# Optimization experiments

Hardware: AMD Instinct MI355X
Metric: run time of the kernel (lower is better)

The kernel has to match this reference:

```python
import jax, jax.numpy as jnp
from jax import lax
import numpy as np

B, N, F_IN, T = 8, 2048, 2, 12
K, F_CHEV, F_TIME = 3, 64, 64
LN_EPS = 1e-5


def _cheb_polys(key):
    # random symmetric row-normalized 'scaled Laplacian' proxy, then Chebyshev recurrence
    A = jax.random.uniform(key, (N, N), dtype=jnp.float32)
    A = (A + A.T) * 0.5
    A = A / A.sum(axis=1, keepdims=True)
    L = A - jnp.eye(N, dtype=jnp.float32)  # eigenvalues roughly in [-1, 1]
    Ts = [jnp.eye(N, dtype=jnp.float32), L]
    for _ in range(2, K):
        Ts.append(2.0 * L @ Ts[-1] - Ts[-2])
    return jnp.stack(Ts[:K])  # (K, N, N)


def setup_inputs() -> dict:
    key = jax.random.key(0)
    ks = jax.random.split(key, 20)
    g = lambda i, s: jax.random.normal(ks[i], s, dtype=jnp.float32)
    xav = lambda i, s: g(i, s) * np.sqrt(2.0 / (s[-2] + s[-1]))
    return {
        "x": g(0, (B, N, F_IN, T)),
        "cheb": _cheb_polys(ks[1]),
        "Theta": xav(2, (K, F_IN, F_CHEV)),
        # temporal attention params
        "U1": g(3, (N,)), "U2": xav(4, (F_IN, N)), "U3": g(5, (F_IN,)),
        "be": g(6, (1, T, T)) * 0.1, "Ve": xav(7, (T, T)),
        # spatial attention params
        "W1": g(8, (T,)), "W2": xav(9, (F_IN, T)), "W3": g(10, (F_IN,)),
        "bs": g(11, (1, N, N)) * 0.1, "Vs": xav(12, (N, N)),
        # convs + layernorm
        "tconv_w": g(13, (F_TIME, F_CHEV, 1, 3)) * np.sqrt(2.0 / (F_CHEV * 3 + F_TIME)),
        "tconv_b": jax.random.uniform(ks[14], (F_TIME,), dtype=jnp.float32),
        "rconv_w": g(15, (F_TIME, F_IN, 1, 1)) * np.sqrt(2.0 / (F_IN + F_TIME)),
        "rconv_b": jax.random.uniform(ks[16], (F_TIME,), dtype=jnp.float32),
        "ln_g": jnp.ones((F_TIME,), jnp.float32),
        "ln_b": jnp.zeros((F_TIME,), jnp.float32),
    }


def _forward(x, cheb, Theta, U1, U2, U3, be, Ve, W1, W2, W3, bs, Vs,
             tconv_w, tconv_b, rconv_w, rconv_b, ln_g, ln_b):
    b, n, f, t = x.shape
    # ---- temporal attention: (B,T,T) ----
    lhs_t = jnp.einsum('bnft,n->btf', x, U1) @ U2          # (B,T,N)
    rhs_t = jnp.einsum('f,bnft->bnt', U3, x)               # (B,N,T)
    prod_t = jnp.einsum('btn,bnu->btu', lhs_t, rhs_t)      # (B,T,T)
    E = jnp.einsum('tu,buv->btv', Ve, jax.nn.sigmoid(prod_t + be))
    E = jax.nn.softmax(E, axis=1)
    # apply temporal attention
    x_TAt = (x.reshape(b, n * f, t) @ E).reshape(b, n, f, t)
    # ---- spatial attention: (B,N,N) ----
    lhs_s = jnp.einsum('bnft,t->bnf', x_TAt, W1) @ W2      # (B,N,T)
    rhs_s = jnp.einsum('f,bnft->btn', W3, x_TAt)           # (B,T,N)
    prod_s = jnp.einsum('bnt,btm->bnm', lhs_s, rhs_s)      # (B,N,N)
    S = jnp.einsum('mn,bnp->bmp', Vs, jax.nn.sigmoid(prod_s + bs))
    S = jax.nn.softmax(S, axis=1)
    # ---- Chebyshev graph conv with spatial attention (vectorized over k, t) ----
    # rhs[b,k,n,f,t] = sum_m (cheb[k,m,n] * S[b,m,n]) * x[b,m,f,t]
    rhs = jnp.einsum('kmn,bmn,bmft->bknft', cheb, S, x)
    gcn = jax.nn.relu(jnp.einsum('bknft,kfo->bnot', rhs, Theta))  # (B,N,F_chev,T)
    # ---- time conv (1x3, pad 1 along T) + 1x1 residual conv ----
    dn = ('NCHW', 'OIHW', 'NCHW')
    tc = lax.conv_general_dilated(gcn.transpose(0, 2, 1, 3), tconv_w, (1, 1),
                                  ((0, 0), (1, 1)), dimension_numbers=dn)
    tc = tc + tconv_b[None, :, None, None]                 # (B,F_time,N,T)
    res = lax.conv_general_dilated(x.transpose(0, 2, 1, 3), rconv_w, (1, 1),
                                   ((0, 0), (0, 0)), dimension_numbers=dn)
    res = res + rconv_b[None, :, None, None]
    y = jax.nn.relu(res + tc).transpose(0, 3, 2, 1)        # (B,T,N,F_time)
    mu = y.mean(-1, keepdims=True)
    var = jnp.mean((y - mu) ** 2, axis=-1, keepdims=True)
    y = (y - mu) * lax.rsqrt(var + LN_EPS) * ln_g + ln_b
    return y.transpose(0, 2, 3, 1)                          # (B,N,F_time,T)


def reference(x, cheb, Theta, U1, U2, U3, be, Ve, W1, W2, W3, bs, Vs,
              tconv_w, tconv_b, rconv_w, rconv_b, ln_g, ln_b):
    return _forward(x, cheb, Theta, U1, U2, U3, be, Ve, W1, W2, W3, bs, Vs,
                    tconv_w, tconv_b, rconv_w, rconv_b, ln_g, ln_b)
```

## Files before the change

### kernel.cpp

```cpp
#include <hip/hip_runtime.h>
#include <cstdint>
#include <cstddef>

#define NB 8
#define NN 2048
#define MCV 16

using bf16x8 = __attribute__((ext_vector_type(8))) __bf16;
using f32x4  = __attribute__((ext_vector_type(4))) float;

__device__ __forceinline__ float bf2f(unsigned short u) {
  union { unsigned int i; float f; } v; v.i = ((unsigned int)u) << 16; return v.f;
}
__device__ __forceinline__ unsigned short f2bf(float f) {
  union { float f; unsigned int i; } v; v.f = f;
  unsigned int lsb = (v.i >> 16) & 1u;
  v.i += 0x7fffu + lsb;
  return (unsigned short)(v.i >> 16);
}
__device__ __forceinline__ float ld_in(const void* p, size_t idx, int mode) {
  return mode ? bf2f(((const unsigned short*)p)[idx]) : ((const float*)p)[idx];
}
__device__ __forceinline__ int get_mode(const void* chebp) {
  return ((const unsigned int*)chebp)[0] != 0x3F800000u;
}

#define GLOAD16(gptr, lptr) \
  __builtin_amdgcn_global_load_lds((const __attribute__((address_space(1))) void*)(gptr), \
                                   (__attribute__((address_space(3))) void*)(lptr), 16, 0, 0)

struct Seg { const void* src; void* dst; int count; int tobf; };
struct ConvArgs { Seg s[16]; };

__global__ void k_convert(ConvArgs a, const void* __restrict__ chebp) {
  const int mode = get_mode(chebp);
  const int stride = gridDim.x * blockDim.x;
  for (int si = 0; si < 16; ++si) {
    const Seg sg = a.s[si];
    for (int i = blockIdx.x * blockDim.x + threadIdx.x; i < sg.count; i += stride) {
      float v = ld_in(sg.src, i, mode);
      if (sg.tobf) ((unsigned short*)sg.dst)[i] = f2bf(v);
      else         ((float*)sg.dst)[i] = v;
    }
  }
}

__global__ void k_vsb(const void* __restrict__ vs, unsigned short* __restrict__ out,
                      const void* __restrict__ tw, unsigned short* __restrict__ twr,
                      const void* __restrict__ chebp) {
  const int mode = get_mode(chebp);
  const int idx = blockIdx.x * 256 + threadIdx.x;
  if (idx < NN * NN) {
    const int ke = idx & 7, row = (idx >> 3) & 127, kc = (idx >> 10) & 7;
    const int hf = (idx >> 13) & 1, kt = (idx >> 14) & 31, mt = idx >> 19;
    const int m = mt * 256 + hf * 128 + row, k = kt * 64 + kc * 8 + ke;
    out[idx] = f2bf(ld_in(vs, (size_t)m * NN + k, mode));
  } else {
    const int j = idx - NN * NN;
    if (j < 12288) {
      const int dt = j >> 12, rem = j & 4095, o = rem >> 6, c = rem & 63;
      twr[j] = f2bf(ld_in(tw, (size_t)o * 192 + c * 3 + dt, mode));
    }
  }
}

__global__ __launch_bounds__(256) void k_temp1(const float* __restrict__ xf,
      const float* __restrict__ U1f, const float* __restrict__ U2f, const float* __restrict__ U3f,
      const float* __restrict__ bef, const float* __restrict__ Vef, float* __restrict__ E) {
  const int b = blockIdx.x;
  float accL[24], accG[24];
#pragma unroll
  for (int i = 0; i < 24; i++) { accL[i] = 0.f; accG[i] = 0.f; }
  const float u30 = U3f[0], u31 = U3f[1];
  for (int n = threadIdx.x; n < NN; n += 256) {
    const float* xp = xf + ((size_t)b * NN + n) * 24;
    const float u1 = U1f[n], u20 = U2f[n], u21 = U2f[NN + n];
#pragma unroll
    for (int t = 0; t < 12; t++) {
      float x0 = xp[t], x1 = xp[12 + t];
      accL[t * 2 + 0] += u1 * x0;
      accL[t * 2 + 1] += u1 * x1;
      float xs = u30 * x0 + u31 * x1;
      accG[t]      += u20 * xs;
      accG[12 + t] += u21 * xs;
    }
  }
#pragma unroll
  for (int i = 0; i < 24; i++) {
#pragma unroll
    for (int d = 32; d >= 1; d >>= 1) {
      accL[i] += __shfl_xor(accL[i], d, 64);
      accG[i] += __shfl_xor(accG[i], d, 64);
    }
  }
  __shared__ float red[4][48];
  __shared__ float L[48];
  __shared__ float s0[12][12], e1[12][12];
  const int lane = threadIdx.x & 63, wv = threadIdx.x >> 6;
  if (lane == 0) {
#pragma unroll
    for (int i = 0; i < 24; i++) { red[wv][i] = accL[i]; red[wv][24 + i] = accG[i]; }
  }
  __syncthreads();
  if (threadIdx.x < 48)
    L[threadIdx.x] = red[0][threadIdx.x] + red[1][threadIdx.x]
                   + red[2][threadIdx.x] + red[3][threadIdx.x];
  __syncthreads();
  const int tid = threadIdx.x;
  const int t = tid / 12, v = tid % 12;
  if (tid < 144) {
    float pr = L[t * 2 + 0] * L[24 + v] + L[t * 2 + 1] * L[36 + v] + bef[t * 12 + v];
    s0[t][v] = 1.f / (1.f + __expf(-pr));
  }
  __syncthreads();
  if (tid < 144) {
    float s = 0.f;
#pragma unroll
    for (int u = 0; u < 12; u++) s += Vef[t * 12 + u] * s0[u][v];
    e1[t][v] = s;
  }
  __syncthreads();
  if (tid < 144) {
    float mx = -1e30f;
#pragma unroll
    for (int u = 0; u < 12; u++) mx = fmaxf(mx, e1[u][v]);
    float sm = 0.f;
#pragma unroll
    for (int u = 0; u < 12; u++) sm += __expf(e1[u][v] - mx);
    E[b * 144 + t * 12 + v] = __expf(e1[t][v] - mx) / sm;
  }
}

__global__ __launch_bounds__(256) void k_xtat(const float* __restrict__ xf,
      const float* __restrict__ E, const float* __restrict__ W1f, const float* __restrict__ W2f,
      const float* __restrict__ W3f, float* __restrict__ lhs, float* __restrict__ rhsS) {
  const int b = blockIdx.y;
  const int n = blockIdx.x * 256 + threadIdx.x;
  __shared__ float Es[144];
  if (threadIdx.x < 144) Es[threadIdx.x] = E[b * 144 + threadIdx.x];
  __syncthreads();
  const float* xp = xf + ((size_t)b * NN + n) * 24;
  float xv[24];
#pragma unroll
  for (int i = 0; i < 24; i++) xv[i] = xp[i];
  float xT[24];
#pragma unroll
  for (int f = 0; f < 2; f++)
#pragma unroll
    for (int v = 0; v < 12; v++) {
      float s = 0.f;
#pragma unroll
      for (int u = 0; u < 12; u++) s += xv[f * 12 + u] * Es[u * 12 + v];
      xT[f * 12 + v] = s;
    }
  float a0 = 0.f, a1 = 0.f;
#pragma unroll
  for (int v = 0; v < 12; v++) { a0 += xT[v] * W1f[v]; a1 += xT[12 + v] * W1f[v]; }
  const float w30 = W3f[0], w31 = W3f[1];
  float* lp = lhs + ((size_t)b * NN + n) * 12;
#pragma unroll
  for (int t = 0; t < 12; t++) {
    lp[t] = a0 * W2f[t] + a1 * W2f[12 + t];
    rhsS[((size_t)b * 12 + t) * NN + n] = w30 * xT[t] + w31 * xT[12 + t];
  }
}

__global__ __launch_bounds__(256) void k_sig(const float* __restrict__ lhs,
      const float* __restrict__ rhsS, const void* __restrict__ bs,
      unsigned short* __restrict__ sigT, const void* __restrict__ chebp, int p0, int PL) {
  const int tid = threadIdx.x;
  const int n = blockIdx.x * 256 + tid;
  const int pg0 = p0 + blockIdx.y * 16;
  const int mode = get_mode(chebp);
  __shared__ float rsl[8][12][16];
  for (int i = tid; i < 1536; i += 256) {
    int b = i / 192, t = (i % 192) / 16, c = i % 16;
    rsl[b][t][c] = rhsS[((size_t)b * 12 + t) * NN + pg0 + c];
  }
  float bsv[16];
  if (mode) {
    const int4* bp = (const int4*)((const unsigned short*)bs + (size_t)n * NN + pg0);
    int4 q0 = bp[0], q1 = bp[1];
    const unsigned short* u0 = (const unsigned short*)&q0;
    const unsigned short* u1 = (const unsigned short*)&q1;
#pragma unroll
    for (int i = 0; i < 8; i++) { bsv[i] = bf2f(u0[i]); bsv[8 + i] = bf2f(u1[i]); }
  } else {
    const float4* fp = (const float4*)((const float*)bs + (size_t)n * NN + pg0);
#pragma unroll
    for (int q = 0; q < 4; q++) {
      float4 v = fp[q];
      bsv[q * 4 + 0] = v.x; bsv[q * 4 + 1] = v.y; bsv[q * 4 + 2] = v.z; bsv[q * 4 + 3] = v.w;
    }
  }
  __syncthreads();
  const size_t kpart = (size_t)(n >> 6) * 16384 + (size_t)((n >> 3) & 7) * 1024 + (n & 7);
  const int plbase = pg0 - p0;
  for (int b = 0; b < 8; b++) {
    float lv[12];
    const float* lp = lhs + ((size_t)b * NN + n) * 12;
#pragma unroll
    for (int t = 0; t < 12; t++) lv[t] = lp[t];
    const int gbase = b * PL + plbase;
    const size_t gt_off = (size_t)(gbase >> 8) * 524288 + (size_t)((gbase >> 7) & 1) * 8192
                        + (size_t)(gbase & 127) * 8;
#pragma unroll
    for (int pp = 0; pp < 16; pp++) {
      float acc = bsv[pp];
#pragma unroll
      for (int t = 0; t < 12; t++) acc += lv[t] * rsl[b][t][pp];
      float sg = 1.f / (1.f + __expf(-acc));
      sigT[gt_off + (size_t)pp * 8 + kpart] = f2bf(sg);
    }
  }
}

__global__ __launch_bounds__(512, 2) void k_gemm(const unsigned short* __restrict__ A,
      const unsigned short* __restrict__ Bm, unsigned short* __restrict__ C,
      float* __restrict__ pmax, float* __restrict__ psum,
      int PL, int plshift, int GP, int nwg) {
  __shared__ __align__(16) unsigned short lA[2][16384];
  __shared__ __align__(16) unsigned short lB[2][16384];
  const int id = blockIdx.x;
  const int cpx = nwg >> 3;
  const int sid = (id & 7) * cpx + (id >> 3);
  const int s = sid >> 4, w = sid & 15;
  const int mt = (s & 1) * 4 + (w & 3);
  const int pt = (s >> 1) * 4 + (w >> 2);
  const int tid = threadIdx.x;
  const int wv = tid >> 6, lane = tid & 63;
  const int fr = lane & 15, hi = lane >> 4;
  const int wr = wv >> 2, wc = wv & 3;
  const unsigned short* gA = A  + (size_t)mt * 524288;
  const unsigned short* gB = Bm + (size_t)pt * 524288;

  f32x4 acc[8][4] = {};
  bf16x8 af[8][2], bfr[4][2];

#define STAGE_H(h) do { \
    const int kt_ = (h) >> 2, part_ = (h) & 3, r_ = part_ & 1; \
    const unsigned short* gsrc_ = ((part_ < 2) ? gA : gB) + (size_t)kt_ * 16384 + r_ * 8192 + tid * 8; \
    unsigned short* ldst_ = ((part_ < 2) ? &lA[0][0] : &lB[0][0]) + (kt_ & 1) * 16384 + r_ * 8192 + wv * 512; \
    GLOAD16(gsrc_,        ldst_); \
    GLOAD16(gsrc_ + 4096, ldst_ + 4096); \
  } while (0)

#define READ_A(bf) do { \
    _Pragma("unroll") for (int mi_ = 0; mi_ < 8; ++mi_) \
    _Pragma("unroll") for (int s2_ = 0; s2_ < 2; ++s2_) \
      af[mi_][s2_] = *(const bf16x8*)&lA[bf][wr * 8192 + (s2_ * 4 + hi) * 1024 + (mi_ * 16 + fr) * 8]; \
  } while (0)

#define READ_B(bf) do { \
    _Pragma("unroll") for (int ni_ = 0; ni_ < 4; ++ni_) \
    _Pragma("unroll") for (int s2_ = 0; s2_ < 2; ++s2_) \
      bfr[ni_][s2_] = *(const bf16x8*)&lB[bf][(wc >> 1) * 8192 + (s2_ * 4 + hi) * 1024 \
                                             + ((wc & 1) * 64 + ni_ * 16 + fr) * 8]; \
  } while (0)

#define MFMA_Q(mh, nh) do { \
    __builtin_amdgcn_s_setprio(1); \
    _Pragma("unroll") for (int s2_ = 0; s2_ < 2; ++s2_) \
    _Pragma("unroll") for (int mi_ = 0; mi_ < 4; ++mi_) \
    _Pragma("unroll") for (int ni_ = 0; ni_ < 2; ++ni_) \
      acc[(mh) * 4 + mi_][(nh) * 2 + ni_] = __builtin_amdgcn_mfma_f32_16x16x32_bf16( \
          af[(mh) * 4 + mi_][s2_], bfr[(nh) * 2 + ni_][s2_], acc[(mh) * 4 + mi_][(nh) * 2 + ni_], 0, 0, 0); \
    __builtin_amdgcn_s_setprio(0); \
  } while (0)

#define PH_BAR() __builtin_amdgcn_s_barrier()
#define PH_LGKM() asm volatile("s_waitcnt lgkmcnt(0)" ::: "memory")

  for (int h = 0; h < 8; ++h) STAGE_H(h);
  asm volatile("s_waitcnt vmcnt(8)" ::: "memory");
  PH_BAR();

#pragma unroll 1
  for (int i = 0; i < 16; ++i) {
    const int hb = 8 * i;
    const bool more = (i < 15);
    READ_A(0); READ_B(0);
    if (i > 0) STAGE_H(hb + 7);
    PH_BAR(); PH_LGKM();
    MFMA_Q(0, 0);
    PH_BAR();
    if (more) STAGE_H(hb + 8);
    PH_BAR(); PH_LGKM();
    MFMA_Q(0, 1);
    PH_BAR();
    if (more) STAGE_H(hb + 9);
    PH_BAR(); PH_LGKM();
    MFMA_Q(1, 0);
    PH_BAR();
    if (more) STAGE_H(hb + 10);
    PH_BAR(); PH_LGKM();
    MFMA_Q(1, 1);
    if (more) asm volatile("s_waitcnt vmcnt(6)" ::: "memory");
    else      asm volatile("s_waitcnt vmcnt(0)" ::: "memory");
    PH_BAR();
    READ_A(1); READ_B(1);
    if (more) STAGE_H(hb + 11);
    PH_BAR(); PH_LGKM();
    MFMA_Q(0, 0);
    PH_BAR();
    if (more) STAGE_H(hb + 12);
    PH_BAR(); PH_LGKM();
    MFMA_Q(0, 1);
    PH_BAR();
    if (more) STAGE_H(hb + 13);
    PH_BAR(); PH_LGKM();
    MFMA_Q(1, 0);
    PH_BAR();
    if (more) STAGE_H(hb + 14);
    PH_BAR(); PH_LGKM();
    MFMA_Q(1, 1);
    if (more) asm volatile("s_waitcnt vmcnt(6)" ::: "memory");
    else      asm volatile("s_waitcnt vmcnt(0)" ::: "memory");
    PH_BAR();
  }
#undef STAGE_H
#undef READ_A
#undef READ_B
#undef MFMA_Q
#undef PH_BAR
#undef PH_LGKM

  const int m0 = mt * 256, gcol0 = pt * 256;
  const int plmask = PL - 1;
#pragma unroll
  for (int ni = 0; ni < 4; ++ni) {
    float lmax = -1e30f;
    float vr[8][4];
#pragma unroll
    for (int mi = 0; mi < 8; ++mi) {
      const int g = gcol0 + wc * 64 + ni * 16 + fr;
      const int b = g >> plshift, pl = g & plmask;
      const int mrow = m0 + wr * 128 + mi * 16 + hi * 4;
      unsigned short* cp = C + ((size_t)b * NN + mrow) * PL + pl;
#pragma unroll
      for (int r = 0; r < 4; r++) {
        unsigned short us = f2bf(acc[mi][ni][r]);
        cp[(size_t)r * PL] = us;
        vr[mi][r] = bf2f(us);
        lmax = fmaxf(lmax, vr[mi][r]);
      }
    }
    float lsum = 0.f;
#pragma unroll
    for (int mi = 0; mi < 8; ++mi)
#pragma unroll
      for (int r = 0; r < 4; r++) lsum += __expf(vr[mi][r] - lmax);
#pragma unroll
    for (int d = 16; d <= 32; d <<= 1) {
      float omax = __shfl_xor(lmax, d, 64);
      float osum = __shfl_xor(lsum, d, 64);
      float nm = fmaxf(lmax, omax);
      lsum = lsum * __expf(lmax - nm) + osum * __expf(omax - nm);
      lmax = nm;
    }
    if (hi == 0) {
      const int part = mt * 2 + wr;
      const int g = gcol0 + wc * 64 + ni * 16 + lane;
      pmax[(size_t)part * GP + g] = lmax;
      psum[(size_t)part * GP + g] = lsum;
    }
  }
}

__global__ __launch_bounds__(256) void k_cheb(const unsigned short* __restrict__ S0c,
        const void* __restrict__ cheb, const unsigned short* __restrict__ cbf, int use_cbf,
        const float* __restrict__ xf, const float* __restrict__ pmax, const float* __restrict__ psum,
        float* __restrict__ part, int p0, int PL, int mspan, int GP) {
  const int b = blockIdx.z, mc = blockIdx.y;
  const int pl = blockIdx.x * 256 + threadIdx.x;
  const int n = p0 + pl;
  const int mode = get_mode(cheb);
  const int g = b * PL + pl;
  float mx = -1e30f;
#pragma unroll
  for (int c = 0; c < 16; c++) mx = fmaxf(mx, pmax[(size_t)c * GP + g]);
  float sm = 0.f;
#pragma unroll
  for (int c = 0; c < 16; c++) sm += psum[(size_t)c * GP + g] * __expf(pmax[(size_t)c * GP + g] - mx);
  const float inv = 1.f / sm;
  float acc[3][24];
#pragma unroll
  for (int k = 0; k < 3; k++)
#pragma unroll
    for (int j = 0; j < 24; j++) acc[k][j] = 0.f;
  const unsigned short* s0p = S0c + (size_t)b * NN * PL + pl;
  const int mEnd = mc * mspan + mspan;
  if (use_cbf || mode) {
    const unsigned short* cb = (use_cbf ? cbf : (const unsigned short*)cheb) + n;
#pragma unroll 2
    for (int m = mc * mspan; m < mEnd; ++m) {
      float w = __expf(bf2f(s0p[(size_t)m * PL]) - mx) * inv;
      const f32x4* xp = (const f32x4*)(xf + ((size_t)b * NN + m) * 24);
      float w0 = w * bf2f(cb[(size_t)m * NN]);
      float w1 = w * bf2f(cb[(size_t)NN * NN + (size_t)m * NN]);
      float w2 = w * bf2f(cb[(size_t)2 * NN * NN + (size_t)m * NN]);
#pragma unroll
      for (int q = 0; q < 6; q++) {
        f32x4 xv = xp[q];
#pragma unroll
        for (int e = 0; e < 4; e++) {
          int j = q * 4 + e;
          acc[0][j] += w0 * xv[e];
          acc[1][j] += w1 * xv[e];
          acc[2][j] += w2 * xv[e];
        }
      }
    }
  } else {
    const float* cb = (const float*)cheb + n;
#pragma unroll 2
    for (int m = mc * mspan; m < mEnd; ++m) {
      float w = __expf(bf2f(s0p[(size_t)m * PL]) - mx) * inv;
      const f32x4* xp = (const f32x4*)(xf + ((size_t)b * NN + m) * 24);
      float w0 = w * cb[(size_t)m * NN];
      float w1 = w * cb[(size_t)NN * NN + (size_t)m * NN];
      float w2 = w * cb[(size_t)2 * NN * NN + (size_t)m * NN];
#pragma unroll
      for (int q = 0; q < 6; q++) {
        f32x4 xv = xp[q];
#pragma unroll
        for (int e = 0; e < 4; e++) {
          int j = q * 4 + e;
          acc[0][j] += w0 * xv[e];
          acc[1][j] += w1 * xv[e];
          acc[2][j] += w2 * xv[e];
        }
      }
    }
  }
  float* pp = part + ((size_t)(mc * 8 + b) * 72) * PL + pl;
#pragma unroll
  for (int k = 0; k < 3; k++)
#pragma unroll
    for (int j = 0; j < 24; j++) pp[(size_t)(k * 24 + j) * PL] = acc[k][j];
}

__global__ void k_chebred(const float* __restrict__ part, float* __restrict__ rhsC,
                          int p0, int PL) {
  const int idx = blockIdx.x * 256 + threadIdx.x;
  if (idx >= 8 * 72 * PL) return;
  const int pl = idx % PL;
  const int r = idx / PL;
  const int j = r % 72, b = r / 72;
  float s = 0.f;
  for (int mc = 0; mc < MCV; ++mc)
    s += part[((size_t)(mc * 8 + b) * 72 + j) * PL + pl];
  rhsC[((size_t)b * NN + p0 + pl) * 72 + j] = s;
}

__global__ __launch_bounds__(256) void k_final(const float* __restrict__ rhsC,
      const float* __restrict__ Thf, const unsigned short* __restrict__ twr,
      const float* __restrict__ tbf, const float* __restrict__ rwf, const float* __restrict__ rbf,
      const float* __restrict__ lngf, const float* __restrict__ lnbf,
      const float* __restrict__ xf, void* __restrict__ out, const void* __restrict__ chebp) {
  const int mode = get_mode(chebp);
  __shared__ __align__(16) unsigned short ltw[192 * 72];
  __shared__ __align__(16) unsigned short gT[4][18][72];
  __shared__ float rl[4][72];
  __shared__ float prm[6][64];
  const int tid = threadIdx.x;
  const int wv = tid >> 6, lane = tid & 63;
  const size_t bn = (size_t)blockIdx.x * 4 + wv;

  for (int i = tid; i < 1536; i += 256) {
    const int row = i >> 3, cseg = (i & 7) * 8;
    *(bf16x8*)&ltw[row * 72 + cseg] = *(const bf16x8*)&twr[row * 64 + cseg];
  }
  if (tid < 64) {
    prm[0][tid] = tbf[tid] + rbf[tid];
    prm[1][tid] = rwf[tid * 2];
    prm[2][tid] = rwf[tid * 2 + 1];
    prm[3][tid] = lngf[tid];
    prm[4][tid] = lnbf[tid];
  }
  for (int i = lane; i < 648; i += 64) ((unsigned int*)&gT[wv][0][0])[i] = 0u;
  {
    const float* rp = rhsC + bn * 72;
    rl[wv][lane] = rp[lane];
    if (lane < 8) rl[wv][64 + lane] = rp[64 + lane];
  }
  __syncthreads();
  {
    const int c = lane;
    float th[6];
#pragma unroll
    for (int kf = 0; kf < 6; kf++) th[kf] = Thf[kf * 64 + c];
#pragma unroll
    for (int t = 0; t < 12; t++) {
      float s = 0.f;
#pragma unroll
      for (int kf = 0; kf < 6; kf++) s += rl[wv][kf * 12 + t] * th[kf];
      gT[wv][1 + t][c] = f2bf(fmaxf(s, 0.f));
    }
  }
  __syncthreads();
  const int fr = lane & 15, hi = lane >> 4;
  f32x4 acc4[4] = {};
#pragma unroll
  for (int dt = 0; dt < 3; dt++)
#pragma unroll
    for (int ks = 0; ks < 2; ks++) {
      bf16x8 bfrag = *(const bf16x8*)&gT[wv][fr + dt][ks * 32 + hi * 8];
#pragma unroll
      for (int ot = 0; ot < 4; ot++) {
        bf16x8 afrag = *(const bf16x8*)&ltw[(dt * 64 + ot * 16 + fr) * 72 + ks * 32 + hi * 8];
        acc4[ot] = __builtin_amdgcn_mfma_f32_16x16x32_bf16(afrag, bfrag, acc4[ot], 0, 0, 0);
      }
    }
  const int t = fr;
  const int tc = t < 12 ? t : 11;
  const float x0 = xf[bn * 24 + tc], x1 = xf[bn * 24 + 12 + tc];
  float vals[4][4];
  float sum = 0.f, sumsq = 0.f;
#pragma unroll
  for (int ot = 0; ot < 4; ot++) {
    f32x4 rbt4 = *(const f32x4*)&prm[0][ot * 16 + hi * 4];
    f32x4 rw04 = *(const f32x4*)&prm[1][ot * 16 + hi * 4];
    f32x4 rw14 = *(const f32x4*)&prm[2][ot * 16 + hi * 4];
#pragma unroll
    for (int r = 0; r < 4; r++) {
      float v = acc4[ot][r] + rbt4[r] + rw04[r] * x0 + rw14[r] * x1;
      v = fmaxf(v, 0.f);
      vals[ot][r] = v;
      sum += v; sumsq += v * v;
    }
  }
  sum   += __shfl_xor(sum, 16, 64);
  sumsq += __shfl_xor(sumsq, 16, 64);
  sum   += __shfl_xor(sum, 32, 64);
  sumsq += __shfl_xor(sumsq, 32, 64);
  const float mu = sum * (1.f / 64.f);
  const float var = sumsq * (1.f / 64.f) - mu * mu;
  const float rs = rsqrtf(var + 1e-5f);
  if (t < 12) {
#pragma unroll
    for (int ot = 0; ot < 4; ot++) {
      f32x4 lg4 = *(const f32x4*)&prm[3][ot * 16 + hi * 4];
      f32x4 lb4 = *(const f32x4*)&prm[4][ot * 16 + hi * 4];
#pragma unroll
      for (int r = 0; r < 4; r++) {
        const int o = ot * 16 + hi * 4 + r;
        float y = (vals[ot][r] - mu) * rs * lg4[r] + lb4[r];
        if (mode) ((unsigned short*)out)[bn * 768 + o * 12 + t] = f2bf(y);
        else      ((float*)out)[bn * 768 + o * 12 + t] = y;
      }
    }
  }
}

struct Plan {
  size_t o_xf, o_Th, o_U1, o_U2, o_U3, o_be, o_Ve, o_W1, o_W2, o_W3,
         o_twr, o_tb, o_rw, o_rb, o_lg, o_lb, o_Vs,
         o_E, o_lhs, o_rhsS, o_rhsC,
         o_R1, o_S0, o_pmax, o_psum, o_cbf;
  size_t total;
};

static Plan make_plan(int PL, int cbf) {
  Plan p; size_t off = 0;
  auto al = [&](size_t b) { size_t r = off; off += (b + 255) & ~(size_t)255; return r; };
  const int GP = 8 * PL;
  p.o_xf   = al((size_t)NB * NN * 24 * 4);
  p.o_Th   = al(384 * 4);
  p.o_U1   = al(2048 * 4);
  p.o_U2   = al(4096 * 4);
  p.o_U3   = al(2 * 4);
  p.o_be   = al(144 * 4);
  p.o_Ve   = al(144 * 4);
  p.o_W1   = al(12 * 4);
  p.o_W2   = al(24 * 4);
  p.o_W3   = al(2 * 4);
  p.o_twr  = al(12288 * 2);
  p.o_tb   = al(64 * 4);
  p.o_rw   = al(128 * 4);
  p.o_rb   = al(64 * 4);
  p.o_lg   = al(64 * 4);
  p.o_lb   = al(64 * 4);
  p.o_Vs   = al((size_t)NN * NN * 2);
  p.o_E    = al(NB * 144 * 4);
  p.o_lhs  = al((size_t)NB * NN * 12 * 4);
  p.o_rhsS = al((size_t)NB * 12 * NN * 4);
  p.o_rhsC = al((size_t)NB * NN * 72 * 4);
  p.o_R1   = al((size_t)36864 * PL);
  p.o_S0   = al((size_t)NB * NN * PL * 2);
  p.o_pmax = al((size_t)16 * GP * 4);
  p.o_psum = al((size_t)16 * GP * 4);
  p.o_cbf  = cbf ? al((size_t)3 * NN * NN * 2) : 0;
  p.total = off;
  return p;
}

extern "C" void kernel_launch(void* const* d_in, const int* in_sizes, int n_in,
                              void* d_out, int out_size, void* d_ws, size_t ws_size,
                              hipStream_t stream) {
  (void)in_sizes; (void)n_in; (void)out_size;
  char* ws = (char*)d_ws;

  int PL, use_cbf;
  if      (make_plan(1024, 1).total <= ws_size) { PL = 1024; use_cbf = 1; }
  else if (make_plan(1024, 0).total <= ws_size) { PL = 1024; use_cbf = 0; }
  else if (make_plan(512, 1).total  <= ws_size) { PL = 512;  use_cbf = 1; }
  else                                          { PL = 512;  use_cbf = 0; }
  const Plan P = make_plan(PL, use_cbf);
  const int GP = 8 * PL;
  const int plshift = (PL == 512) ? 9 : 10;
  const int mspan = NN / MCV;
  const void* chebp = d_in[1];

  float* xf   = (float*)(ws + P.o_xf);
  float* Ebuf = (float*)(ws + P.o_E);
  float* lhs  = (float*)(ws + P.o_lhs);
  float* rhsS = (float*)(ws + P.o_rhsS);
  float* rhsC = (float*)(ws + P.o_rhsC);
  unsigned short* sigT = (unsigned short*)(ws + P.o_R1);
  float* part = (float*)(ws + P.o_R1);
  unsigned short* S0c  = (unsigned short*)(ws + P.o_S0);
  float* pmax = (float*)(ws + P.o_pmax);
  float* psum = (float*)(ws + P.o_psum);
  unsigned short* cbfp = use_cbf ? (unsigned short*)(ws + P.o_cbf)
                                 : (unsigned short*)d_in[1];

  ConvArgs ca;
  auto seg = [&](int i, int di, size_t o, int count, int tobf) {
    ca.s[i].src = d_in[di]; ca.s[i].dst = (void*)(ws + o); ca.s[i].count = count; ca.s[i].tobf = tobf;
  };
  seg(0, 0, P.o_xf, 393216, 0);
  seg(1, 2, P.o_Th, 384, 0);
  seg(2, 3, P.o_U1, 2048, 0);
  seg(3, 4, P.o_U2, 4096, 0);
  seg(4, 5, P.o_U3, 2, 0);
  seg(5, 6, P.o_be, 144, 0);
  seg(6, 7, P.o_Ve, 144, 0);
  seg(7, 8, P.o_W1, 12, 0);
  seg(8, 9, P.o_W2, 24, 0);
  seg(9, 10, P.o_W3, 2, 0);
  seg(10, 14, P.o_tb, 64, 0);
  seg(11, 15, P.o_rw, 128, 0);
  seg(12, 16, P.o_rb, 64, 0);
  seg(13, 17, P.o_lg, 64, 0);
  seg(14, 18, P.o_lb, 64, 0);
  seg(15, 1, P.o_cbf, use_cbf ? 3 * NN * NN : 0, 1);
  k_convert<<<1024, 256, 0, stream>>>(ca, chebp);
  k_vsb<<<(NN * NN + 12288 + 255) / 256, 256, 0, stream>>>(d_in[12],
      (unsigned short*)(ws + P.o_Vs), d_in[13], (unsigned short*)(ws + P.o_twr), chebp);

  k_temp1<<<NB, 256, 0, stream>>>(xf, (float*)(ws + P.o_U1), (float*)(ws + P.o_U2),
                                  (float*)(ws + P.o_U3), (float*)(ws + P.o_be),
                                  (float*)(ws + P.o_Ve), Ebuf);
  k_xtat<<<dim3(8, NB), 256, 0, stream>>>(xf, Ebuf, (float*)(ws + P.o_W1), (float*)(ws + P.o_W2),
                                          (float*)(ws + P.o_W3), lhs, rhsS);

  const int nwg = 8 * (GP / 256);
  for (int p0 = 0; p0 < NN; p0 += PL) {
    k_sig<<<dim3(8, PL / 16), 256, 0, stream>>>(lhs, rhsS, d_in[11], sigT, chebp, p0, PL);
    k_gemm<<<nwg, 512, 0, stream>>>((unsigned short*)(ws + P.o_Vs), sigT, S0c,
                                    pmax, psum, PL, plshift, GP, nwg);
    k_cheb<<<dim3(PL / 256, MCV, NB), 256, 0, stream>>>(S0c, d_in[1], cbfp, use_cbf,
                                                        xf, pmax, psum, part, p0, PL, mspan, GP);
    k_chebred<<<(8 * 72 * PL + 255) / 256, 256, 0, stream>>>(part, rhsC, p0, PL);
  }

  k_final<<<NB * NN / 4, 256, 0, stream>>>(rhsC, (float*)(ws + P.o_Th),
      (unsigned short*)(ws + P.o_twr), (float*)(ws + P.o_tb), (float*)(ws + P.o_rw),
      (float*)(ws + P.o_rb), (float*)(ws + P.o_lg), (float*)(ws + P.o_lb), xf, d_out, chebp);
}
```

Measured before the change: 373.8 us.

## Split LDS fragment reads across MFMA phases and store Chebyshev partials as bf16

The GEMM main loop now reads A and B fragments from LDS in halves, just before the MFMA quarter that uses them, instead of all at once. The global staging order and vmcnt thresholds are reshuffled so the next tiles are prefetched earlier relative to their use. Separately, the per-chunk Chebyshev partial sums are written and reduced as bf16 rather than fp32, which halves that buffer's traffic and shrinks the workspace region. The bf16 partials lose precision in the 16-way reduction, and the new staging order has to stay consistent with the LDS double buffering.

```diff
diff --git a/kernel.cpp b/kernel.cpp
--- a/kernel.cpp
+++ b/kernel.cpp
@@ -245,14 +245,27 @@
     GLOAD16(gsrc_ + 4096, ldst_ + 4096); \
   } while (0)
 
-#define READ_A(bf) do { \
-    _Pragma("unroll") for (int mi_ = 0; mi_ < 8; ++mi_) \
+#define READ_A03(bf) do { \
+    _Pragma("unroll") for (int mi_ = 0; mi_ < 4; ++mi_) \
     _Pragma("unroll") for (int s2_ = 0; s2_ < 2; ++s2_) \
       af[mi_][s2_] = *(const bf16x8*)&lA[bf][wr * 8192 + (s2_ * 4 + hi) * 1024 + (mi_ * 16 + fr) * 8]; \
   } while (0)
 
-#define READ_B(bf) do { \
-    _Pragma("unroll") for (int ni_ = 0; ni_ < 4; ++ni_) \
+#define READ_A47(bf) do { \
+    _Pragma("unroll") for (int mi_ = 4; mi_ < 8; ++mi_) \
+    _Pragma("unroll") for (int s2_ = 0; s2_ < 2; ++s2_) \
+      af[mi_][s2_] = *(const bf16x8*)&lA[bf][wr * 8192 + (s2_ * 4 + hi) * 1024 + (mi_ * 16 + fr) * 8]; \
+  } while (0)
+
+#define READ_B01(bf) do { \
+    _Pragma("unroll") for (int ni_ = 0; ni_ < 2; ++ni_) \
+    _Pragma("unroll") for (int s2_ = 0; s2_ < 2; ++s2_) \
+      bfr[ni_][s2_] = *(const bf16x8*)&lB[bf][(wc >> 1) * 8192 + (s2_ * 4 + hi) * 1024 \
+                                             + ((wc & 1) * 64 + ni_ * 16 + fr) * 8]; \
+  } while (0)
+
+#define READ_B23(bf) do { \
+    _Pragma("unroll") for (int ni_ = 2; ni_ < 4; ++ni_) \
     _Pragma("unroll") for (int s2_ = 0; s2_ < 2; ++s2_) \
       bfr[ni_][s2_] = *(const bf16x8*)&lB[bf][(wc >> 1) * 8192 + (s2_ * 4 + hi) * 1024 \
                                              + ((wc & 1) * 64 + ni_ * 16 + fr) * 8]; \
@@ -279,48 +292,54 @@
   for (int i = 0; i < 16; ++i) {
     const int hb = 8 * i;
     const bool more = (i < 15);
-    READ_A(0); READ_B(0);
-    if (i > 0) STAGE_H(hb + 7);
+    READ_A03(0); READ_B01(0);
+    if (i > 0) STAGE_H(hb + 4);
     PH_BAR(); PH_LGKM();
     MFMA_Q(0, 0);
     PH_BAR();
+    READ_B23(0);
+    if (i > 0) STAGE_H(hb + 5);
+    PH_BAR(); PH_LGKM();
+    MFMA_Q(0, 1);
+    PH_BAR();
+    READ_A47(0);
+    if (more) STAGE_H(hb + 10);
+    PH_BAR(); PH_LGKM();
+    MFMA_Q(1, 0);
+    PH_BAR();
+    if (more) STAGE_H(hb + 11);
+    PH_BAR(); PH_LGKM();
+    MFMA_Q(1, 1);
+    if (more || i == 0) asm volatile("s_waitcnt vmcnt(4)" ::: "memory");
+    else                asm volatile("s_waitcnt vmcnt(0)" ::: "memory");
+    PH_BAR();
+    READ_A03(1); READ_B01(1);
     if (more) STAGE_H(hb + 8);
     PH_BAR(); PH_LGKM();
+    MFMA_Q(0, 0);
+    PH_BAR();
+    READ_B23(1);
+    if (more) STAGE_H(hb + 9);
+    PH_BAR(); PH_LGKM();
     MFMA_Q(0, 1);
     PH_BAR();
-    if (more) STAGE_H(hb + 9);
+    READ_A47(1);
+    if (more) STAGE_H(hb + 14);
     PH_BAR(); PH_LGKM();
     MFMA_Q(1, 0);
     PH_BAR();
-    if (more) STAGE_H(hb + 10);
+    if (more) STAGE_H(hb + 15);
     PH_BAR(); PH_LGKM();
     MFMA_Q(1, 1);
-    if (more) asm volatile("s_waitcnt vmcnt(6)" ::: "memory");
+    if (more) asm volatile("s_waitcnt vmcnt(4)" ::: "memory");
     else      asm volatile("s_waitcnt vmcnt(0)" ::: "memory");
     PH_BAR();
-    READ_A(1); READ_B(1);
-    if (more) STAGE_H(hb + 11);
-    PH_BAR(); PH_LGKM();
-    MFMA_Q(0, 0);
-    PH_BAR();
-    if (more) STAGE_H(hb + 12);
-    PH_BAR(); PH_LGKM();
-    MFMA_Q(0, 1);
-    PH_BAR();
-    if (more) STAGE_H(hb + 13);
-    PH_BAR(); PH_LGKM();
-    MFMA_Q(1, 0);
-    PH_BAR();
-    if (more) STAGE_H(hb + 14);
-    PH_BAR(); PH_LGKM();
-    MFMA_Q(1, 1);
-    if (more) asm volatile("s_waitcnt vmcnt(6)" ::: "memory");
-    else      asm volatile("s_waitcnt vmcnt(0)" ::: "memory");
-    PH_BAR();
   }
 #undef STAGE_H
-#undef READ_A
-#undef READ_B
+#undef READ_A03
+#undef READ_A47
+#undef READ_B01
+#undef READ_B23
 #undef MFMA_Q
 #undef PH_BAR
 #undef PH_LGKM
@@ -370,7 +389,7 @@
 __global__ __launch_bounds__(256) void k_cheb(const unsigned short* __restrict__ S0c,
         const void* __restrict__ cheb, const unsigned short* __restrict__ cbf, int use_cbf,
         const float* __restrict__ xf, const float* __restrict__ pmax, const float* __restrict__ psum,
-        float* __restrict__ part, int p0, int PL, int mspan, int GP) {
+        unsigned short* __restrict__ part, int p0, int PL, int mspan, int GP) {
   const int b = blockIdx.z, mc = blockIdx.y;
   const int pl = blockIdx.x * 256 + threadIdx.x;
   const int n = p0 + pl;
@@ -433,14 +452,14 @@
       }
     }
   }
-  float* pp = part + ((size_t)(mc * 8 + b) * 72) * PL + pl;
+  unsigned short* pp = part + ((size_t)(mc * 8 + b) * 72) * PL + pl;
 #pragma unroll
   for (int k = 0; k < 3; k++)
 #pragma unroll
-    for (int j = 0; j < 24; j++) pp[(size_t)(k * 24 + j) * PL] = acc[k][j];
-}
-
-__global__ void k_chebred(const float* __restrict__ part, float* __restrict__ rhsC,
+    for (int j = 0; j < 24; j++) pp[(size_t)(k * 24 + j) * PL] = f2bf(acc[k][j]);
+}
+
+__global__ void k_chebred(const unsigned short* __restrict__ part, float* __restrict__ rhsC,
                           int p0, int PL) {
   const int idx = blockIdx.x * 256 + threadIdx.x;
   if (idx >= 8 * 72 * PL) return;
@@ -449,7 +468,7 @@
   const int j = r % 72, b = r / 72;
   float s = 0.f;
   for (int mc = 0; mc < MCV; ++mc)
-    s += part[((size_t)(mc * 8 + b) * 72 + j) * PL + pl];
+    s += bf2f(part[((size_t)(mc * 8 + b) * 72 + j) * PL + pl]);
   rhsC[((size_t)b * NN + p0 + pl) * 72 + j] = s;
 }
 
@@ -586,7 +605,7 @@
   p.o_lhs  = al((size_t)NB * NN * 12 * 4);
   p.o_rhsS = al((size_t)NB * 12 * NN * 4);
   p.o_rhsC = al((size_t)NB * NN * 72 * 4);
-  p.o_R1   = al((size_t)36864 * PL);
+  p.o_R1   = al((size_t)32768 * PL);
   p.o_S0   = al((size_t)NB * NN * PL * 2);
   p.o_pmax = al((size_t)16 * GP * 4);
   p.o_psum = al((size_t)16 * GP * 4);
@@ -618,7 +637,7 @@
   float* rhsS = (float*)(ws + P.o_rhsS);
   float* rhsC = (float*)(ws + P.o_rhsC);
   unsigned short* sigT = (unsigned short*)(ws + P.o_R1);
-  float* part = (float*)(ws + P.o_R1);
+  unsigned short* part = (unsigned short*)(ws + P.o_R1);
   unsigned short* S0c  = (unsigned short*)(ws + P.o_S0);
   float* pmax = (float*)(ws + P.o_pmax);
   float* psum = (float*)(ws + P.o_psum);
```

After: 361.4 us. -3.3%, faster.
